# Kernel optimization log

Measured on AMD Instinct MI355X. Metric: run time of the kernel, lower is better.

## Reference

```python
import jax, jax.numpy as jnp
import numpy as np

NUM_HEADS = 16


def _bayes_w(mu, rho, eps):
    # reparameterized weight sample: w = mu + softplus(rho) * eps
    return mu + jax.nn.softplus(rho) * eps


def setup_inputs() -> dict:
    key = jax.random.key(0)
    ks = jax.random.split(key, 12)
    B, N, C = 4, 2048, 1024
    x = jax.random.normal(ks[0], (B, N, C), jnp.float32)
    w_scale = 0.02
    q_w = jax.random.normal(ks[1], (C, C), jnp.float32) * w_scale
    k_w = jax.random.normal(ks[2], (C, C), jnp.float32) * w_scale
    v_mu = jax.random.normal(ks[3], (C, C), jnp.float32) * w_scale
    v_rho = jax.random.normal(ks[4], (C, C), jnp.float32) * 0.1 - 3.0
    v_eps = jax.random.normal(ks[5], (C, C), jnp.float32)
    proj_mu = jax.random.normal(ks[6], (C, C), jnp.float32) * w_scale
    proj_rho = jax.random.normal(ks[7], (C, C), jnp.float32) * 0.1 - 3.0
    proj_eps = jax.random.normal(ks[8], (C, C), jnp.float32)
    pb_mu = jax.random.normal(ks[9], (C,), jnp.float32) * w_scale
    pb_rho = jax.random.normal(ks[10], (C,), jnp.float32) * 0.1 - 3.0
    pb_eps = jax.random.normal(ks[11], (C,), jnp.float32)
    return {"x": x, "q_w": q_w, "k_w": k_w, "v_mu": v_mu, "v_rho": v_rho,
            "v_eps": v_eps, "proj_mu": proj_mu, "proj_rho": proj_rho,
            "proj_eps": proj_eps, "pb_mu": pb_mu, "pb_rho": pb_rho,
            "pb_eps": pb_eps}


def reference(x, q_w, k_w, v_mu, v_rho, v_eps, proj_mu, proj_rho, proj_eps,
              pb_mu, pb_rho, pb_eps):
    B, N, C = x.shape
    H = NUM_HEADS
    D = C // H
    scale = D ** -0.5
    v_w = _bayes_w(v_mu, v_rho, v_eps)
    # projections (torch Linear: y = x @ W.T)
    q = (x @ q_w.T).reshape(B, N, H, D).transpose(0, 2, 1, 3)  # [B,H,N,D]
    k = (x @ k_w.T).reshape(B, N, H, D).transpose(0, 2, 1, 3)
    v = (x @ v_w.T).reshape(B, N, H, D).transpose(0, 2, 1, 3)
    attn = jax.nn.softmax(jnp.einsum("bhnd,bhmd->bhnm", q * scale, k), axis=-1)
    out = jnp.einsum("bhnm,bhmd->bhnd", attn, v)
    out = out.transpose(0, 2, 1, 3).reshape(B, N, C)
    p_w = _bayes_w(proj_mu, proj_rho, proj_eps)
    p_b = _bayes_w(pb_mu, pb_rho, pb_eps)
    return out @ p_w.T + p_b
```

## Files before the change

### kernel.cpp

```cpp
#include <hip/hip_runtime.h>
#include <hip/hip_bf16.h>
#include <cstdint>
#include <math.h>

typedef __bf16 bf16;
typedef __bf16 bf16x8 __attribute__((ext_vector_type(8)));
typedef __bf16 bf16x4 __attribute__((ext_vector_type(4)));
typedef float  f32x4 __attribute__((ext_vector_type(4)));

#define LOG2E 1.4426950408889634f

#if __has_builtin(__builtin_amdgcn_exp2f)
#define EXP2(x) __builtin_amdgcn_exp2f(x)
#else
#define EXP2(x) exp2f(x)
#endif

#define AS1 __attribute__((address_space(1)))
#define AS3 __attribute__((address_space(3)))

__device__ __forceinline__ void gload_lds16(const bf16* g, bf16* l) {
    __builtin_amdgcn_global_load_lds((AS1 void*)g, (AS3 void*)l, 16, 0, 0);
}

__global__ __launch_bounds__(256)
void cast_f32_bf16(const float* __restrict__ in, bf16* __restrict__ out, int n4) {
    int i = blockIdx.x * 256 + threadIdx.x;
    if (i < n4) {
        float4 v = ((const float4*)in)[i];
        bf16 o[4] = {(bf16)v.x, (bf16)v.y, (bf16)v.z, (bf16)v.w};
        *(uint64_t*)&((bf16*)out)[i * 4] = *(uint64_t*)o;
    }
}

__global__ __launch_bounds__(256)
void bayes_w_kernel(const float* __restrict__ mu, const float* __restrict__ rho,
                    const float* __restrict__ eps, bf16* __restrict__ out, int n) {
    int i = blockIdx.x * 256 + threadIdx.x;
    if (i < n) {
        float r = rho[i];
        float sp = (r > 15.f) ? r : log1pf(expf(r));
        out[i] = (bf16)(mu[i] + sp * eps[i]);
    }
}

__global__ __launch_bounds__(256)
void bayes_b_kernel(const float* __restrict__ mu, const float* __restrict__ rho,
                    const float* __restrict__ eps, float* __restrict__ out, int n) {
    int i = blockIdx.x * 256 + threadIdx.x;
    if (i < n) {
        float r = rho[i];
        float sp = (r > 15.f) ? r : log1pf(expf(r));
        out[i] = mu[i] + sp * eps[i];
    }
}

template <typename OutT>
__global__ __launch_bounds__(256)
void gemm_bt(const bf16* __restrict__ A, const bf16* __restrict__ W,
             OutT* __restrict__ C, const float* __restrict__ bias,
             int M, int N, int K, float q_scale, int q_cols) {
    __shared__ bf16 lA[128 * 32];
    __shared__ bf16 lB[128 * 32];

    const int lane = threadIdx.x & 63;
    const int wv   = threadIdx.x >> 6;
    const int wr   = wv >> 1, wc = wv & 1;
    const int m0 = blockIdx.y * 128, n0 = blockIdx.x * 128;
    const int col = lane & 15, quad = lane >> 4;
    const float scale = (n0 < q_cols) ? q_scale : 1.0f;

    const int srow  = wv * 16 + (lane >> 2);
    const int skcol = (lane & 3) * 8;

    f32x4 acc[4][4] = {};

    for (int k0 = 0; k0 < K; k0 += 32) {
#pragma unroll
        for (int r = 0; r < 2; ++r) {
            gload_lds16(A + (size_t)(m0 + r * 64 + srow) * K + k0 + skcol,
                        &lA[(r * 64 + wv * 16) * 32]);
            gload_lds16(W + (size_t)(n0 + r * 64 + srow) * K + k0 + skcol,
                        &lB[(r * 64 + wv * 16) * 32]);
        }
        __syncthreads();

        bf16x8 af[4], bfr[4];
#pragma unroll
        for (int t = 0; t < 4; ++t) {
            af[t]  = *(const bf16x8*)&lA[(wr * 64 + t * 16 + col) * 32 + quad * 8];
            bfr[t] = *(const bf16x8*)&lB[(wc * 64 + t * 16 + col) * 32 + quad * 8];
        }
#pragma unroll
        for (int i = 0; i < 4; ++i)
#pragma unroll
            for (int j = 0; j < 4; ++j)
                acc[i][j] = __builtin_amdgcn_mfma_f32_16x16x32_bf16(af[i], bfr[j], acc[i][j], 0, 0, 0);
        __syncthreads();
    }

#pragma unroll
    for (int i = 0; i < 4; ++i) {
        int row = m0 + wr * 64 + i * 16 + quad * 4;
#pragma unroll
        for (int j = 0; j < 4; ++j) {
            int cc = n0 + wc * 64 + j * 16 + col;
            float bv = bias ? bias[cc] : 0.f;
#pragma unroll
            for (int r = 0; r < 4; ++r)
                C[(size_t)(row + r) * N + cc] = (OutT)(acc[i][j][r] * scale + bv);
        }
    }
}

__global__ __launch_bounds__(256, 4)
void attn_kernel(const bf16* __restrict__ QKV, bf16* __restrict__ O) {
    __shared__ bf16 sK [64 * 64];
    __shared__ bf16 sVt[64 * 72];
    __shared__ bf16 sP [128 * 72];

    const int lane = threadIdx.x & 63;
    const int wv   = threadIdx.x >> 6;
    const int col  = lane & 15, quad = lane >> 4;
    const int qt = blockIdx.x, h = blockIdx.y, b = blockIdx.z;

    const size_t rowQ0 = (size_t)b * 2048 + qt * 128;
    const bf16* Qg = QKV + rowQ0 * 3072 + h * 64;
    const bf16* Kg = QKV + (size_t)b * 2048 * 3072 + 1024 + h * 64;
    const bf16* Vg = QKV + (size_t)b * 2048 * 3072 + 2048 + h * 64;

#pragma unroll
    for (int it = 0; it < 4; ++it) {
        int c = it * 256 + threadIdx.x;
        int row = c >> 3, dc = (c & 7) * 8;
        *(bf16x8*)&sP[row * 72 + dc] = *(const bf16x8*)&Qg[(size_t)row * 3072 + dc];
    }
    __syncthreads();
    bf16x8 qf[2][2];
#pragma unroll
    for (int mi = 0; mi < 2; ++mi)
#pragma unroll
        for (int ks = 0; ks < 2; ++ks)
            qf[mi][ks] = *(const bf16x8*)&sP[(wv * 32 + mi * 16 + col) * 72 + ks * 32 + quad * 8];

    const int rloc = lane >> 3;
    const bf16* Kdma = Kg + (size_t)(wv * 16 + rloc) * 3072 + (((lane & 7) ^ rloc) * 8);

    f32x4 lsum[2] = {};
    f32x4 o[2][4] = {};
    const int cx = col & 7;

    for (int kv0 = 0; kv0 < 2048; kv0 += 64) {
        gload_lds16(Kdma + (size_t)kv0 * 3072,       &sK[(wv * 16) * 64]);
        gload_lds16(Kdma + (size_t)(kv0 + 8) * 3072, &sK[(wv * 16 + 8) * 64]);
#pragma unroll
        for (int it = 0; it < 2; ++it) {
            int c = it * 256 + threadIdx.x;
            int row = c & 63, dc = (c >> 6) * 8;
            bf16x8 v = *(const bf16x8*)&Vg[(size_t)(kv0 + row) * 3072 + dc];
#pragma unroll
            for (int j = 0; j < 8; ++j) sVt[(dc + j) * 72 + row] = v[j];
        }
        __syncthreads();

        f32x4 st[2][4];
#pragma unroll
        for (int nj = 0; nj < 4; ++nj) {
            bf16x8 kf0 = *(const bf16x8*)&sK[(nj * 16 + col) * 64 + ((quad ^ cx) * 8)];
            bf16x8 kf1 = *(const bf16x8*)&sK[(nj * 16 + col) * 64 + (((quad ^ cx) ^ 4) * 8)];
#pragma unroll
            for (int mi = 0; mi < 2; ++mi) {
                f32x4 t = {0.f, 0.f, 0.f, 0.f};
                t = __builtin_amdgcn_mfma_f32_16x16x32_bf16(kf0, qf[mi][0], t, 0, 0, 0);
                t = __builtin_amdgcn_mfma_f32_16x16x32_bf16(kf1, qf[mi][1], t, 0, 0, 0);
                st[mi][nj] = t;
            }
        }

#pragma unroll
        for (int mi = 0; mi < 2; ++mi) {
#pragma unroll
            for (int nj = 0; nj < 4; ++nj) {
                f32x4 p;
#pragma unroll
                for (int r = 0; r < 4; ++r) p[r] = EXP2(st[mi][nj][r]);
                lsum[mi] += p;
                bf16x4 pk = {(bf16)p[0], (bf16)p[1], (bf16)p[2], (bf16)p[3]};
                *(bf16x4*)&sP[(wv * 32 + mi * 16 + col) * 72 + nj * 16 + quad * 4] = pk;
            }
        }

#pragma unroll
        for (int ks = 0; ks < 2; ++ks) {
            bf16x8 pf0 = *(const bf16x8*)&sP[(wv * 32 + col) * 72 + ks * 32 + quad * 8];
            bf16x8 pf1 = *(const bf16x8*)&sP[(wv * 32 + 16 + col) * 72 + ks * 32 + quad * 8];
#pragma unroll
            for (int dj = 0; dj < 4; ++dj) {
                bf16x8 vf = *(const bf16x8*)&sVt[(dj * 16 + col) * 72 + ks * 32 + quad * 8];
                o[0][dj] = __builtin_amdgcn_mfma_f32_16x16x32_bf16(pf0, vf, o[0][dj], 0, 0, 0);
                o[1][dj] = __builtin_amdgcn_mfma_f32_16x16x32_bf16(pf1, vf, o[1][dj], 0, 0, 0);
            }
        }
        __syncthreads();
    }

#pragma unroll
    for (int mi = 0; mi < 2; ++mi) {
        float l = lsum[mi][0] + lsum[mi][1] + lsum[mi][2] + lsum[mi][3];
        l += __shfl_xor(l, 16, 64);
        l += __shfl_xor(l, 32, 64);
#pragma unroll
        for (int r = 0; r < 4; ++r) {
            float inv = 1.f / __shfl(l, quad * 4 + r, 64);
            size_t row = rowQ0 + wv * 32 + mi * 16 + quad * 4 + r;
#pragma unroll
            for (int dj = 0; dj < 4; ++dj)
                O[row * 1024 + h * 64 + dj * 16 + col] = (bf16)(o[mi][dj][r] * inv);
        }
    }
}

extern "C" void kernel_launch(void* const* d_in, const int* in_sizes, int n_in,
                              void* d_out, int out_size, void* d_ws, size_t ws_size,
                              hipStream_t stream) {
    const float* x      = (const float*)d_in[0];
    const float* q_w    = (const float*)d_in[1];
    const float* k_w    = (const float*)d_in[2];
    const float* v_mu   = (const float*)d_in[3];
    const float* v_rho  = (const float*)d_in[4];
    const float* v_eps  = (const float*)d_in[5];
    const float* p_mu   = (const float*)d_in[6];
    const float* p_rho  = (const float*)d_in[7];
    const float* p_eps  = (const float*)d_in[8];
    const float* pb_mu  = (const float*)d_in[9];
    const float* pb_rho = (const float*)d_in[10];
    const float* pb_eps = (const float*)d_in[11];
    float* out = (float*)d_out;

    const size_t MN = (size_t)8192 * 1024;
    const size_t MB = (size_t)1 << 20;
    char* ws = (char*)d_ws;
    bf16*  xb   = (bf16*)(ws);
    bf16*  wqkv = (bf16*)(ws + 16 * MB);
    bf16*  pwb  = (bf16*)(ws + 22 * MB);
    float* p_b  = (float*)(ws + 24 * MB);
    bf16*  QKV  = (bf16*)(ws + 25 * MB);
    bf16*  Ab   = xb;

    const int Wsz = 1024 * 1024;
    cast_f32_bf16<<<(int)(MN / 4 / 256), 256, 0, stream>>>(x, xb, (int)(MN / 4));
    cast_f32_bf16<<<1024, 256, 0, stream>>>(q_w, wqkv, Wsz / 4);
    cast_f32_bf16<<<1024, 256, 0, stream>>>(k_w, wqkv + Wsz, Wsz / 4);
    bayes_w_kernel<<<4096, 256, 0, stream>>>(v_mu, v_rho, v_eps, wqkv + 2 * Wsz, Wsz);
    bayes_w_kernel<<<4096, 256, 0, stream>>>(p_mu, p_rho, p_eps, pwb, Wsz);
    bayes_b_kernel<<<4, 256, 0, stream>>>(pb_mu, pb_rho, pb_eps, p_b, 1024);

    gemm_bt<bf16><<<dim3(24, 64), 256, 0, stream>>>(xb, wqkv, QKV, nullptr,
                                                    8192, 3072, 1024, 0.125f * LOG2E, 1024);

    attn_kernel<<<dim3(16, 16, 4), 256, 0, stream>>>(QKV, Ab);

    gemm_bt<float><<<dim3(8, 64), 256, 0, stream>>>(Ab, pwb, out, p_b,
                                                    8192, 1024, 1024, 1.0f, 1024);
}
```

Measured before the change: 332.3 us.

## Double-buffer K tiles, prefetch V into registers, swizzle LDS, remap workgroups by XCD

```diff
diff --git a/kernel.cpp b/kernel.cpp
--- a/kernel.cpp
+++ b/kernel.cpp
@@ -66,7 +66,12 @@
     const int lane = threadIdx.x & 63;
     const int wv   = threadIdx.x >> 6;
     const int wr   = wv >> 1, wc = wv & 1;
-    const int m0 = blockIdx.y * 128, n0 = blockIdx.x * 128;
+
+    const int nwg = gridDim.x * gridDim.y;
+    int bidl = blockIdx.y * gridDim.x + blockIdx.x;
+    if ((nwg & 7) == 0) bidl = (bidl & 7) * (nwg >> 3) + (bidl >> 3);
+    const int m0 = (bidl / gridDim.x) * 128, n0 = (bidl % gridDim.x) * 128;
+
     const int col = lane & 15, quad = lane >> 4;
     const float scale = (n0 < q_cols) ? q_scale : 1.0f;
 
@@ -113,27 +118,42 @@
     }
 }
 
+#define SWZ(row, ec) ((row) * 64 + ((ec) ^ (((row) & 7) << 3)))
+
 __global__ __launch_bounds__(256, 4)
 void attn_kernel(const bf16* __restrict__ QKV, bf16* __restrict__ O) {
-    __shared__ bf16 sK [64 * 64];
-    __shared__ bf16 sVt[64 * 72];
-    __shared__ bf16 sP [128 * 72];
+    __shared__ bf16 sK[2][64 * 64];
+    __shared__ bf16 sVt[64 * 64];
+    __shared__ bf16 sP [128 * 64];
 
     const int lane = threadIdx.x & 63;
     const int wv   = threadIdx.x >> 6;
     const int col  = lane & 15, quad = lane >> 4;
-    const int qt = blockIdx.x, h = blockIdx.y, b = blockIdx.z;
+
+    const int bid  = blockIdx.x;
+    const int work = (bid & 7) * 128 + (bid >> 3);
+    const int qt = work & 15, h = (work >> 4) & 15, b = work >> 8;
 
     const size_t rowQ0 = (size_t)b * 2048 + qt * 128;
     const bf16* Qg = QKV + rowQ0 * 3072 + h * 64;
     const bf16* Kg = QKV + (size_t)b * 2048 * 3072 + 1024 + h * 64;
     const bf16* Vg = QKV + (size_t)b * 2048 * 3072 + 2048 + h * 64;
 
+    const int rloc = lane >> 3;
+    const bf16* Kdma = Kg + (size_t)(wv * 16 + rloc) * 3072 + (((lane & 7) ^ rloc) * 8);
+
+    gload_lds16(Kdma,                    &sK[0][(wv * 16) * 64]);
+    gload_lds16(Kdma + (size_t)8 * 3072, &sK[0][(wv * 16 + 8) * 64]);
+
+    const int dc0 = wv * 8, dc1 = 32 + wv * 8;
+    bf16x8 vr0 = *(const bf16x8*)&Vg[(size_t)lane * 3072 + dc0];
+    bf16x8 vr1 = *(const bf16x8*)&Vg[(size_t)lane * 3072 + dc1];
+
 #pragma unroll
     for (int it = 0; it < 4; ++it) {
         int c = it * 256 + threadIdx.x;
-        int row = c >> 3, dc = (c & 7) * 8;
-        *(bf16x8*)&sP[row * 72 + dc] = *(const bf16x8*)&Qg[(size_t)row * 3072 + dc];
+        int row = c >> 3, ec = (c & 7) * 8;
+        *(bf16x8*)&sP[SWZ(row, ec)] = *(const bf16x8*)&Qg[(size_t)row * 3072 + ec];
     }
     __syncthreads();
     bf16x8 qf[2][2];
@@ -141,66 +161,75 @@
     for (int mi = 0; mi < 2; ++mi)
 #pragma unroll
         for (int ks = 0; ks < 2; ++ks)
-            qf[mi][ks] = *(const bf16x8*)&sP[(wv * 32 + mi * 16 + col) * 72 + ks * 32 + quad * 8];
-
-    const int rloc = lane >> 3;
-    const bf16* Kdma = Kg + (size_t)(wv * 16 + rloc) * 3072 + (((lane & 7) ^ rloc) * 8);
+            qf[mi][ks] = *(const bf16x8*)&sP[SWZ(wv * 32 + mi * 16 + col, ks * 32 + quad * 8)];
 
     f32x4 lsum[2] = {};
     f32x4 o[2][4] = {};
     const int cx = col & 7;
 
-    for (int kv0 = 0; kv0 < 2048; kv0 += 64) {
-        gload_lds16(Kdma + (size_t)kv0 * 3072,       &sK[(wv * 16) * 64]);
-        gload_lds16(Kdma + (size_t)(kv0 + 8) * 3072, &sK[(wv * 16 + 8) * 64]);
-#pragma unroll
-        for (int it = 0; it < 2; ++it) {
-            int c = it * 256 + threadIdx.x;
-            int row = c & 63, dc = (c >> 6) * 8;
-            bf16x8 v = *(const bf16x8*)&Vg[(size_t)(kv0 + row) * 3072 + dc];
-#pragma unroll
-            for (int j = 0; j < 8; ++j) sVt[(dc + j) * 72 + row] = v[j];
-        }
-        __syncthreads();
+    for (int t = 0; t < 32; ++t) {
+        const int p = t & 1;
+
+#pragma unroll
+        for (int j = 0; j < 8; ++j) sVt[SWZ(dc0 + j, lane)] = vr0[j];
+#pragma unroll
+        for (int j = 0; j < 8; ++j) sVt[SWZ(dc1 + j, lane)] = vr1[j];
+        __syncthreads();
+
+        if (t < 31) {
+            const bf16* kn = Kdma + (size_t)(t * 64 + 64) * 3072;
+            gload_lds16(kn,                    &sK[p ^ 1][(wv * 16) * 64]);
+            gload_lds16(kn + (size_t)8 * 3072, &sK[p ^ 1][(wv * 16 + 8) * 64]);
+        }
 
         f32x4 st[2][4];
+        __builtin_amdgcn_s_setprio(1);
 #pragma unroll
         for (int nj = 0; nj < 4; ++nj) {
-            bf16x8 kf0 = *(const bf16x8*)&sK[(nj * 16 + col) * 64 + ((quad ^ cx) * 8)];
-            bf16x8 kf1 = *(const bf16x8*)&sK[(nj * 16 + col) * 64 + (((quad ^ cx) ^ 4) * 8)];
+            bf16x8 kf0 = *(const bf16x8*)&sK[p][(nj * 16 + col) * 64 + ((quad ^ cx) * 8)];
+            bf16x8 kf1 = *(const bf16x8*)&sK[p][(nj * 16 + col) * 64 + (((quad ^ cx) ^ 4) * 8)];
 #pragma unroll
             for (int mi = 0; mi < 2; ++mi) {
-                f32x4 t = {0.f, 0.f, 0.f, 0.f};
-                t = __builtin_amdgcn_mfma_f32_16x16x32_bf16(kf0, qf[mi][0], t, 0, 0, 0);
-                t = __builtin_amdgcn_mfma_f32_16x16x32_bf16(kf1, qf[mi][1], t, 0, 0, 0);
-                st[mi][nj] = t;
+                f32x4 tacc = {0.f, 0.f, 0.f, 0.f};
+                tacc = __builtin_amdgcn_mfma_f32_16x16x32_bf16(kf0, qf[mi][0], tacc, 0, 0, 0);
+                tacc = __builtin_amdgcn_mfma_f32_16x16x32_bf16(kf1, qf[mi][1], tacc, 0, 0, 0);
+                st[mi][nj] = tacc;
             }
         }
+        __builtin_amdgcn_s_setprio(0);
 
 #pragma unroll
         for (int mi = 0; mi < 2; ++mi) {
 #pragma unroll
             for (int nj = 0; nj < 4; ++nj) {
-                f32x4 p;
-#pragma unroll
-                for (int r = 0; r < 4; ++r) p[r] = EXP2(st[mi][nj][r]);
-                lsum[mi] += p;
-                bf16x4 pk = {(bf16)p[0], (bf16)p[1], (bf16)p[2], (bf16)p[3]};
-                *(bf16x4*)&sP[(wv * 32 + mi * 16 + col) * 72 + nj * 16 + quad * 4] = pk;
+                f32x4 pv;
+#pragma unroll
+                for (int r = 0; r < 4; ++r) pv[r] = EXP2(st[mi][nj][r]);
+                lsum[mi] += pv;
+                bf16x4 pk = {(bf16)pv[0], (bf16)pv[1], (bf16)pv[2], (bf16)pv[3]};
+                *(bf16x4*)&sP[SWZ(wv * 32 + mi * 16 + col, nj * 16 + quad * 4)] = pk;
             }
         }
 
+        if (t < 31) {
+            const bf16* vn = Vg + (size_t)(t * 64 + 64 + lane) * 3072;
+            vr0 = *(const bf16x8*)&vn[dc0];
+            vr1 = *(const bf16x8*)&vn[dc1];
+        }
+
+        __builtin_amdgcn_s_setprio(1);
 #pragma unroll
         for (int ks = 0; ks < 2; ++ks) {
-            bf16x8 pf0 = *(const bf16x8*)&sP[(wv * 32 + col) * 72 + ks * 32 + quad * 8];
-            bf16x8 pf1 = *(const bf16x8*)&sP[(wv * 32 + 16 + col) * 72 + ks * 32 + quad * 8];
+            bf16x8 pf0 = *(const bf16x8*)&sP[SWZ(wv * 32 + col,      ks * 32 + quad * 8)];
+            bf16x8 pf1 = *(const bf16x8*)&sP[SWZ(wv * 32 + 16 + col, ks * 32 + quad * 8)];
 #pragma unroll
             for (int dj = 0; dj < 4; ++dj) {
-                bf16x8 vf = *(const bf16x8*)&sVt[(dj * 16 + col) * 72 + ks * 32 + quad * 8];
+                bf16x8 vf = *(const bf16x8*)&sVt[SWZ(dj * 16 + col, ks * 32 + quad * 8)];
                 o[0][dj] = __builtin_amdgcn_mfma_f32_16x16x32_bf16(pf0, vf, o[0][dj], 0, 0, 0);
                 o[1][dj] = __builtin_amdgcn_mfma_f32_16x16x32_bf16(pf1, vf, o[1][dj], 0, 0, 0);
             }
         }
+        __builtin_amdgcn_s_setprio(0);
         __syncthreads();
     }
 
@@ -258,7 +287,7 @@
     gemm_bt<bf16><<<dim3(24, 64), 256, 0, stream>>>(xb, wqkv, QKV, nullptr,
                                                     8192, 3072, 1024, 0.125f * LOG2E, 1024);
 
-    attn_kernel<<<dim3(16, 16, 4), 256, 0, stream>>>(QKV, Ab);
+    attn_kernel<<<dim3(1024), 256, 0, stream>>>(QKV, Ab);
 
     gemm_bt<float><<<dim3(8, 64), 256, 0, stream>>>(Ab, pwb, out, p_b,
                                                     8192, 1024, 1024, 1.0f, 1024);
```

After: 317.6 us. -4.4%, faster.
